# Performance work log

Hardware: AMD Instinct MI355X
Metric: run time of the kernel (lower is better)

The kernel has to match this reference:

```python
import jax, jax.numpy as jnp
import numpy as np

B, T, D, H = 4, 2048, 1024, 16
HD = D // H  # head_size = 64


def setup_inputs() -> dict:
    key = jax.random.key(0)
    ks = jax.random.split(key, 6)
    s = 0.02
    x = jax.random.normal(ks[0], (B, T, D), dtype=jnp.float32)
    # per-head unfused projections, stacked over heads: [H, D, HD]
    Wq = jax.random.normal(ks[1], (H, D, HD), dtype=jnp.float32) * s
    Wk = jax.random.normal(ks[2], (H, D, HD), dtype=jnp.float32) * s
    Wv = jax.random.normal(ks[3], (H, D, HD), dtype=jnp.float32) * s
    # output projection, torch Linear layout [out, in]
    Wo = jax.random.normal(ks[4], (D, D), dtype=jnp.float32) * s
    bo = jax.random.normal(ks[5], (D,), dtype=jnp.float32) * s
    return {"x": x, "Wq": Wq, "Wk": Wk, "Wv": Wv, "Wo": Wo, "bo": bo}


def reference(x, Wq, Wk, Wv, Wo, bo):
    b, t, d = x.shape
    hd = Wq.shape[-1]
    q = jnp.einsum('btd,hdk->bhtk', x, Wq)
    k = jnp.einsum('btd,hdk->bhtk', x, Wk)
    v = jnp.einsum('btd,hdk->bhtk', x, Wv)
    scores = jnp.einsum('bhtk,bhsk->bhts', q, k) / jnp.sqrt(jnp.float32(hd))
    mask = jnp.tril(jnp.ones((t, t), dtype=bool))  # causal
    scores = jnp.where(mask, scores, jnp.float32(-jnp.inf))
    p = jax.nn.softmax(scores, axis=-1)
    o = jnp.einsum('bhts,bhsk->bhtk', p, v)
    o = o.transpose(0, 2, 1, 3).reshape(b, t, d)  # concat heads
    return o @ Wo.T + bo
```

## Files before the change

### kernel.cpp

```cpp
#include <hip/hip_runtime.h>
#include <hip/hip_bf16.h>
#include <stdint.h>

#define B_   4
#define T_   2048
#define D_   1024
#define H_   16
#define HD_  64
#define MROWS (B_*T_)
#define NQKV  3072
#define NST  (T_/64)

typedef __attribute__((ext_vector_type(8))) short  short8;
typedef __attribute__((ext_vector_type(4))) short  bf16x4;
typedef __attribute__((ext_vector_type(4))) float  floatx4;

#define QSCALE 0.1803368801111244f

__device__ inline void async_copy16(const __hip_bfloat16* g, __hip_bfloat16* l) {
  __builtin_amdgcn_global_load_lds(
      (const __attribute__((address_space(1))) void*)g,
      (__attribute__((address_space(3))) void*)l, 16, 0, 0);
}

__device__ inline floatx4 mfma16(bf16x4 a, bf16x4 b, floatx4 c) {
#if __has_builtin(__builtin_amdgcn_mfma_f32_16x16x16bf16_1k)
  return __builtin_amdgcn_mfma_f32_16x16x16bf16_1k(a, b, c, 0, 0, 0);
#elif __has_builtin(__builtin_amdgcn_mfma_f32_16x16x16_bf16)
  return __builtin_amdgcn_mfma_f32_16x16x16_bf16(a, b, c, 0, 0, 0);
#else
  short8 a8 = (short8){a[0], a[1], a[2], a[3], 0, 0, 0, 0};
  short8 b8 = (short8){b[0], b[1], b[2], b[3], 0, 0, 0, 0};
  return __builtin_amdgcn_mfma_f32_16x16x32_bf16(a8, b8, c, 0, 0, 0);
#endif
}


__global__ void convert_bf16(const float* __restrict__ in, __hip_bfloat16* __restrict__ out, int n) {
  int i = (blockIdx.x * blockDim.x + threadIdx.x) * 4;
  if (i < n) {
    float4 v = *(const float4*)(in + i);
    out[i + 0] = __float2bfloat16(v.x);
    out[i + 1] = __float2bfloat16(v.y);
    out[i + 2] = __float2bfloat16(v.z);
    out[i + 3] = __float2bfloat16(v.w);
  }
}

__global__ void transpose_w(const float* __restrict__ Wq, const float* __restrict__ Wk,
                            const float* __restrict__ Wv, __hip_bfloat16* __restrict__ wqkv) {
  __shared__ __hip_bfloat16 tile[64][65];
  const int t = threadIdx.x;
  const int d0 = blockIdx.x * 64;
  const int wh = blockIdx.y;
  const int which = wh >> 4, h = wh & 15;
  const float* W = (which == 0) ? Wq : ((which == 1) ? Wk : Wv);
  const float* base = W + (size_t)h * D_ * HD_;
#pragma unroll
  for (int i = 0; i < 16; i++) {
    int e = i * 256 + t;
    int dr = e >> 6, hd = e & 63;
    tile[dr][hd] = __float2bfloat16(base[(size_t)(d0 + dr) * HD_ + hd]);
  }
  __syncthreads();
#pragma unroll
  for (int i = 0; i < 16; i++) {
    int e = i * 256 + t;
    int hd = e >> 6, dr = e & 63;
    wqkv[(size_t)(which * 1024 + h * 64 + hd) * D_ + d0 + dr] = tile[dr][hd];
  }
}

__global__ void repack_kv(const __hip_bfloat16* __restrict__ qkv,
                          __hip_bfloat16* __restrict__ kpack, __hip_bfloat16* __restrict__ vpack) {
  __shared__ __hip_bfloat16 Ks[64][72];
  __shared__ __hip_bfloat16 Vs[64][72];
  const int tid = threadIdx.x;
  const int st = blockIdx.x, bh = blockIdx.y;
  const int b = bh >> 4, h = bh & 15;
#pragma unroll
  for (int p = 0; p < 2; p++) {
    int c = p * 256 + tid;
    int row = c >> 3, col8 = c & 7;
    const __hip_bfloat16* src = qkv + (size_t)(b * T_ + st * 64 + row) * NQKV + h * HD_ + col8 * 8;
    *(uint4*)&Ks[row][col8 * 8] = *(const uint4*)(src + 1024);
    *(uint4*)&Vs[row][col8 * 8] = *(const uint4*)(src + 2048);
  }
  __syncthreads();
  const size_t base = ((size_t)bh * NST + st) * 8 * 512;
#pragma unroll
  for (int p = 0; p < 2; p++) {
    int pair = p * 256 + tid;
    int c = pair >> 6, l = pair & 63;
    int lq = l & 15, q = l >> 4;
    int ni = c >> 1, half = c & 1;
    short8 v = *(const short8*)&Ks[ni * 16 + lq][half * 32 + q * 8];
    *(short8*)(kpack + base + (size_t)c * 512 + l * 8) = v;
  }
#pragma unroll
  for (int p = 0; p < 2; p++) {
    int pair = p * 256 + tid;
    int c = pair >> 6, l = pair & 63;
    int lq = l & 15, q = l >> 4;
    int m = c >> 2, nt = c & 3;
    __hip_bfloat16 tmp[8];
#pragma unroll
    for (int half = 0; half < 2; half++)
#pragma unroll
      for (int j = 0; j < 4; j++)
        tmp[half * 4 + j] = Vs[(2 * m + half) * 16 + q * 4 + j][nt * 16 + lq];
    *(short8*)(vpack + base + (size_t)c * 512 + l * 8) = *(short8*)tmp;
  }
}

template <int EPI>
__launch_bounds__(256, 2)
__global__ void gemm_bt(const __hip_bfloat16* __restrict__ A, const __hip_bfloat16* __restrict__ Bt,
                        __hip_bfloat16* __restrict__ Cb, float* __restrict__ Cf,
                        const float* __restrict__ bias, int M, int N, int K, float qscale) {
  __shared__ __hip_bfloat16 As[128 * 32];
  __shared__ __hip_bfloat16 Bs[128 * 32];
  const int tid = threadIdx.x;
  const int w = tid >> 6, lane = tid & 63;
  const int lq = lane & 15, quad = lane >> 4;
  const int wr = w >> 1, wc = w & 1;
  const int m0 = blockIdx.x * 128, n0 = blockIdx.y * 128;

  floatx4 acc[4][4];
#pragma unroll
  for (int i = 0; i < 4; i++)
#pragma unroll
    for (int j = 0; j < 4; j++) acc[i][j] = (floatx4){0.f, 0.f, 0.f, 0.f};

  for (int k0 = 0; k0 < K; k0 += 32) {
    __syncthreads();
#pragma unroll
    for (int ph = 0; ph < 2; ++ph) {
      int c = ph * 256 + tid;
      int row = c >> 2, col8 = c & 3;
      async_copy16(A + (size_t)(m0 + row) * K + k0 + col8 * 8, As + c * 8);
      async_copy16(Bt + (size_t)(n0 + row) * K + k0 + col8 * 8, Bs + c * 8);
    }
    __syncthreads();
    short8 af[4], bf[4];
#pragma unroll
    for (int mi = 0; mi < 4; mi++)
      af[mi] = *(const short8*)(As + (wr * 64 + mi * 16 + lq) * 32 + quad * 8);
#pragma unroll
    for (int ni = 0; ni < 4; ni++)
      bf[ni] = *(const short8*)(Bs + (wc * 64 + ni * 16 + lq) * 32 + quad * 8);
#pragma unroll
    for (int mi = 0; mi < 4; mi++)
#pragma unroll
      for (int ni = 0; ni < 4; ni++)
        acc[mi][ni] = __builtin_amdgcn_mfma_f32_16x16x32_bf16(af[mi], bf[ni], acc[mi][ni], 0, 0, 0);
  }

#pragma unroll
  for (int mi = 0; mi < 4; mi++) {
#pragma unroll
    for (int ni = 0; ni < 4; ni++) {
      int col = n0 + wc * 64 + ni * 16 + lq;
      if (EPI == 0) {
        float s = (col < 1024) ? qscale : 1.0f;
#pragma unroll
        for (int r = 0; r < 4; r++) {
          int row = m0 + wr * 64 + mi * 16 + quad * 4 + r;
          Cb[(size_t)row * N + col] = __float2bfloat16(acc[mi][ni][r] * s);
        }
      } else {
        float bv = bias[col];
#pragma unroll
        for (int r = 0; r < 4; r++) {
          int row = m0 + wr * 64 + mi * 16 + quad * 4 + r;
          Cf[(size_t)row * N + col] = acc[mi][ni][r] + bv;
        }
      }
    }
  }
}

__launch_bounds__(256, 4)
__global__ void attn(const __hip_bfloat16* __restrict__ qkv,
                     const __hip_bfloat16* __restrict__ kpack,
                     const __hip_bfloat16* __restrict__ vpack,
                     __hip_bfloat16* __restrict__ obuf) {
  const int tid = threadIdx.x;
  const int w = tid >> 6, lane = tid & 63;
  const int lq = lane & 15, quad = lane >> 4;

  const int L = (int)(blockIdx.x + gridDim.x * blockIdx.y);
  const int bh = (L & 7) * 8 + ((L >> 3) & 7);
  const int qpair = L >> 6;
  const int b = bh >> 4, h = bh & 15;

  const __hip_bfloat16* kb0 = kpack + ((size_t)bh * NST) * 4096 + lane * 8;
  const __hip_bfloat16* vb0 = vpack + ((size_t)bh * NST) * 4096 + lane * 8;

#pragma unroll 1
  for (int seg = 0; seg < 2; ++seg) {
    const int qt = seg ? (NST - 1 - qpair) : qpair;
    const int qt0 = qt * 64;

    short8 qf0, qf1;
    {
      const __hip_bfloat16* qp = qkv + ((size_t)(b * T_ + qt0 + w * 16 + lq)) * NQKV + h * HD_;
      qf0 = *(const short8*)(qp + quad * 8);
      qf1 = *(const short8*)(qp + 32 + quad * 8);
    }

    floatx4 Oacc[4];
#pragma unroll
    for (int i = 0; i < 4; i++) Oacc[i] = (floatx4){0.f, 0.f, 0.f, 0.f};
    float lrow = 0.f;

    const __hip_bfloat16* kb = kb0;
    const __hip_bfloat16* vb = vb0;
    const int nIter = qt + 1;
    for (int it = 0; it < nIter; ++it) {
      short8 kf[4], kg[4];
#pragma unroll
      for (int ni = 0; ni < 4; ni++) {
        kf[ni] = *(const short8*)(kb + (size_t)(ni * 2 + 0) * 512);
        kg[ni] = *(const short8*)(kb + (size_t)(ni * 2 + 1) * 512);
      }
      short8 vfr[8];
#pragma unroll
      for (int c = 0; c < 8; c++) vfr[c] = *(const short8*)(vb + (size_t)c * 512);

      floatx4 Sc[4];
#pragma unroll
      for (int ni = 0; ni < 4; ni++) {
        floatx4 c0 = (floatx4){0.f, 0.f, 0.f, 0.f};
        c0 = __builtin_amdgcn_mfma_f32_16x16x32_bf16(kf[ni], qf0, c0, 0, 0, 0);
        c0 = __builtin_amdgcn_mfma_f32_16x16x32_bf16(kg[ni], qf1, c0, 0, 0, 0);
        Sc[ni] = c0;
      }

      if (it == nIter - 1) {
#pragma unroll
        for (int ni = 0; ni < 4; ni++)
#pragma unroll
          for (int r = 0; r < 4; r++) {
            int s_loc = ni * 16 + quad * 4 + r;
            if (s_loc > w * 16 + lq) Sc[ni][r] = -__builtin_inff();
          }
      }

      bf16x4 pf[4];
#pragma unroll
      for (int c = 0; c < 4; c++) {
        __hip_bfloat16 pb[4];
#pragma unroll
        for (int r = 0; r < 4; r++) {
          float p = __builtin_amdgcn_exp2f(Sc[c][r]);
          lrow += p;
          pb[r] = __float2bfloat16(p);
        }
        pf[c] = *(bf16x4*)pb;
      }

#pragma unroll
      for (int m = 0; m < 2; m++)
#pragma unroll
        for (int nt = 0; nt < 4; nt++) {
          short8 v8 = vfr[m * 4 + nt];
          bf16x4 vlo = (bf16x4){v8[0], v8[1], v8[2], v8[3]};
          bf16x4 vhi = (bf16x4){v8[4], v8[5], v8[6], v8[7]};
          Oacc[nt] = mfma16(pf[2 * m + 0], vlo, Oacc[nt]);
          Oacc[nt] = mfma16(pf[2 * m + 1], vhi, Oacc[nt]);
        }

      kb += 4096;
      vb += 4096;
    }

    float ps = lrow;
    ps += __shfl_xor(ps, 16);
    ps += __shfl_xor(ps, 32);
    float inv = 1.0f / ps;
#pragma unroll
    for (int r = 0; r < 4; r++) {
      float invr = __shfl(inv, quad * 4 + r);
      int t = qt0 + w * 16 + quad * 4 + r;
#pragma unroll
      for (int nt = 0; nt < 4; nt++)
        obuf[(size_t)(b * T_ + t) * D_ + h * HD_ + nt * 16 + lq] =
            __float2bfloat16(Oacc[nt][r] * invr);
    }
  }
}


extern "C" void kernel_launch(void* const* d_in, const int* in_sizes, int n_in,
                              void* d_out, int out_size, void* d_ws, size_t ws_size,
                              hipStream_t stream) {
  const float* x  = (const float*)d_in[0];
  const float* Wq = (const float*)d_in[1];
  const float* Wk = (const float*)d_in[2];
  const float* Wv = (const float*)d_in[3];
  const float* Wo = (const float*)d_in[4];
  const float* bo = (const float*)d_in[5];
  float* out = (float*)d_out;

  char* ws = (char*)d_ws;
  __hip_bfloat16* xb    = (__hip_bfloat16*)(ws);
  __hip_bfloat16* obuf  = (__hip_bfloat16*)(ws);
  __hip_bfloat16* wqkv  = (__hip_bfloat16*)(ws + ((size_t)16 << 20));
  __hip_bfloat16* wob   = (__hip_bfloat16*)(ws + ((size_t)22 << 20));
  __hip_bfloat16* qkv   = (__hip_bfloat16*)(ws + ((size_t)24 << 20));
  __hip_bfloat16* kpack = (__hip_bfloat16*)(ws + ((size_t)72 << 20));
  __hip_bfloat16* vpack = (__hip_bfloat16*)(ws + ((size_t)88 << 20));

  convert_bf16<<<(MROWS * D_) / 1024, 256, 0, stream>>>(x, xb, MROWS * D_);
  convert_bf16<<<(D_ * D_) / 1024, 256, 0, stream>>>(Wo, wob, D_ * D_);
  transpose_w<<<dim3(16, 48), 256, 0, stream>>>(Wq, Wk, Wv, wqkv);

  gemm_bt<0><<<dim3(MROWS / 128, NQKV / 128), 256, 0, stream>>>(
      xb, wqkv, qkv, nullptr, nullptr, MROWS, NQKV, D_, QSCALE);

  repack_kv<<<dim3(NST, B_ * H_), 256, 0, stream>>>(qkv, kpack, vpack);

  attn<<<dim3(NST / 2, B_ * H_), 256, 0, stream>>>(qkv, kpack, vpack, obuf);

  gemm_bt<1><<<dim3(MROWS / 128, D_ / 128), 256, 0, stream>>>(
      obuf, wob, nullptr, out, bo, MROWS, D_, D_, 1.0f);
}
```

Baseline: 267.7 us.

## Give each attention wave two 16-row query blocks to reuse K/V fragments

Each wave now handles 32 query rows (two 16-row blocks) instead of 16, so every K/V fragment loaded from global memory feeds twice as many MFMAs. A block covers two adjacent 64-row query tiles, one per wave pair, instead of a front/back pair of tiles processed in sequence. This drops the causal load-balancing pairing and the bh swizzle, and reverses blockIdx.x so the longest tiles launch first. Register pressure rises, so the launch bound is lowered from 4 to 3 waves per SIMD, and the two wave pairs in a block now do unequal work.

Result: slower. 292.5 us (+9.2%).

```diff
diff --git a/kernel.cpp b/kernel.cpp
--- a/kernel.cpp
+++ b/kernel.cpp
@@ -180,7 +180,7 @@
   }
 }
 
-__launch_bounds__(256, 4)
+__launch_bounds__(256, 3)
 __global__ void attn(const __hip_bfloat16* __restrict__ qkv,
                      const __hip_bfloat16* __restrict__ kpack,
                      const __hip_bfloat16* __restrict__ vpack,
@@ -189,104 +189,115 @@
   const int w = tid >> 6, lane = tid & 63;
   const int lq = lane & 15, quad = lane >> 4;
 
-  const int L = (int)(blockIdx.x + gridDim.x * blockIdx.y);
-  const int bh = (L & 7) * 8 + ((L >> 3) & 7);
-  const int qpair = L >> 6;
+  const int j = 15 - (int)blockIdx.x;
+  const int bh = blockIdx.y;
   const int b = bh >> 4, h = bh & 15;
-
-  const __hip_bfloat16* kb0 = kpack + ((size_t)bh * NST) * 4096 + lane * 8;
-  const __hip_bfloat16* vb0 = vpack + ((size_t)bh * NST) * 4096 + lane * 8;
-
-#pragma unroll 1
-  for (int seg = 0; seg < 2; ++seg) {
-    const int qt = seg ? (NST - 1 - qpair) : qpair;
-    const int qt0 = qt * 64;
-
-    short8 qf0, qf1;
-    {
-      const __hip_bfloat16* qp = qkv + ((size_t)(b * T_ + qt0 + w * 16 + lq)) * NQKV + h * HD_;
-      qf0 = *(const short8*)(qp + quad * 8);
-      qf1 = *(const short8*)(qp + 32 + quad * 8);
-    }
-
-    floatx4 Oacc[4];
-#pragma unroll
-    for (int i = 0; i < 4; i++) Oacc[i] = (floatx4){0.f, 0.f, 0.f, 0.f};
-    float lrow = 0.f;
-
-    const __hip_bfloat16* kb = kb0;
-    const __hip_bfloat16* vb = vb0;
-    const int nIter = qt + 1;
-    for (int it = 0; it < nIter; ++it) {
-      short8 kf[4], kg[4];
-#pragma unroll
-      for (int ni = 0; ni < 4; ni++) {
-        kf[ni] = *(const short8*)(kb + (size_t)(ni * 2 + 0) * 512);
-        kg[ni] = *(const short8*)(kb + (size_t)(ni * 2 + 1) * 512);
-      }
-      short8 vfr[8];
-#pragma unroll
-      for (int c = 0; c < 8; c++) vfr[c] = *(const short8*)(vb + (size_t)c * 512);
-
-      floatx4 Sc[4];
+  const int qt = 2 * j + (w >> 1);
+  const int rbase = (w & 1) * 32;
+
+  short8 qf[2][2];
+#pragma unroll
+  for (int bi = 0; bi < 2; bi++) {
+    const __hip_bfloat16* qp =
+        qkv + ((size_t)(b * T_ + qt * 64 + rbase + bi * 16 + lq)) * NQKV + h * HD_;
+    qf[bi][0] = *(const short8*)(qp + quad * 8);
+    qf[bi][1] = *(const short8*)(qp + 32 + quad * 8);
+  }
+
+  floatx4 Oacc[2][4];
+#pragma unroll
+  for (int bi = 0; bi < 2; bi++)
+#pragma unroll
+    for (int i = 0; i < 4; i++) Oacc[bi][i] = (floatx4){0.f, 0.f, 0.f, 0.f};
+  float lrow[2] = {0.f, 0.f};
+
+  const __hip_bfloat16* kb = kpack + ((size_t)bh * NST) * 4096 + lane * 8;
+  const __hip_bfloat16* vb = vpack + ((size_t)bh * NST) * 4096 + lane * 8;
+
+  const int nIter = qt + 1;
+  for (int it = 0; it < nIter; ++it) {
+    short8 kf[4], kg[4];
+#pragma unroll
+    for (int ni = 0; ni < 4; ni++) {
+      kf[ni] = *(const short8*)(kb + (size_t)(ni * 2 + 0) * 512);
+      kg[ni] = *(const short8*)(kb + (size_t)(ni * 2 + 1) * 512);
+    }
+    short8 vfr[8];
+#pragma unroll
+    for (int c = 0; c < 8; c++) vfr[c] = *(const short8*)(vb + (size_t)c * 512);
+
+    floatx4 Sc[2][4];
+#pragma unroll
+    for (int bi = 0; bi < 2; bi++)
 #pragma unroll
       for (int ni = 0; ni < 4; ni++) {
         floatx4 c0 = (floatx4){0.f, 0.f, 0.f, 0.f};
-        c0 = __builtin_amdgcn_mfma_f32_16x16x32_bf16(kf[ni], qf0, c0, 0, 0, 0);
-        c0 = __builtin_amdgcn_mfma_f32_16x16x32_bf16(kg[ni], qf1, c0, 0, 0, 0);
-        Sc[ni] = c0;
-      }
-
-      if (it == nIter - 1) {
+        c0 = __builtin_amdgcn_mfma_f32_16x16x32_bf16(kf[ni], qf[bi][0], c0, 0, 0, 0);
+        c0 = __builtin_amdgcn_mfma_f32_16x16x32_bf16(kg[ni], qf[bi][1], c0, 0, 0, 0);
+        Sc[bi][ni] = c0;
+      }
+
+    if (it == nIter - 1) {
+#pragma unroll
+      for (int bi = 0; bi < 2; bi++) {
+        int lrow_idx = rbase + bi * 16 + lq;
 #pragma unroll
         for (int ni = 0; ni < 4; ni++)
 #pragma unroll
           for (int r = 0; r < 4; r++) {
             int s_loc = ni * 16 + quad * 4 + r;
-            if (s_loc > w * 16 + lq) Sc[ni][r] = -__builtin_inff();
+            if (s_loc > lrow_idx) Sc[bi][ni][r] = -__builtin_inff();
           }
       }
-
-      bf16x4 pf[4];
+    }
+
+    bf16x4 pf[2][4];
+#pragma unroll
+    for (int bi = 0; bi < 2; bi++)
 #pragma unroll
       for (int c = 0; c < 4; c++) {
         __hip_bfloat16 pb[4];
 #pragma unroll
         for (int r = 0; r < 4; r++) {
-          float p = __builtin_amdgcn_exp2f(Sc[c][r]);
-          lrow += p;
+          float p = __builtin_amdgcn_exp2f(Sc[bi][c][r]);
+          lrow[bi] += p;
           pb[r] = __float2bfloat16(p);
         }
-        pf[c] = *(bf16x4*)pb;
-      }
-
-#pragma unroll
-      for (int m = 0; m < 2; m++)
-#pragma unroll
-        for (int nt = 0; nt < 4; nt++) {
-          short8 v8 = vfr[m * 4 + nt];
-          bf16x4 vlo = (bf16x4){v8[0], v8[1], v8[2], v8[3]};
-          bf16x4 vhi = (bf16x4){v8[4], v8[5], v8[6], v8[7]};
-          Oacc[nt] = mfma16(pf[2 * m + 0], vlo, Oacc[nt]);
-          Oacc[nt] = mfma16(pf[2 * m + 1], vhi, Oacc[nt]);
+        pf[bi][c] = *(bf16x4*)pb;
+      }
+
+#pragma unroll
+    for (int m = 0; m < 2; m++)
+#pragma unroll
+      for (int nt = 0; nt < 4; nt++) {
+        short8 v8 = vfr[m * 4 + nt];
+        bf16x4 vlo = (bf16x4){v8[0], v8[1], v8[2], v8[3]};
+        bf16x4 vhi = (bf16x4){v8[4], v8[5], v8[6], v8[7]};
+#pragma unroll
+        for (int bi = 0; bi < 2; bi++) {
+          Oacc[bi][nt] = mfma16(pf[bi][2 * m + 0], vlo, Oacc[bi][nt]);
+          Oacc[bi][nt] = mfma16(pf[bi][2 * m + 1], vhi, Oacc[bi][nt]);
         }
-
-      kb += 4096;
-      vb += 4096;
-    }
-
-    float ps = lrow;
+      }
+
+    kb += 4096;
+    vb += 4096;
+  }
+
+#pragma unroll
+  for (int bi = 0; bi < 2; bi++) {
+    float ps = lrow[bi];
     ps += __shfl_xor(ps, 16);
     ps += __shfl_xor(ps, 32);
     float inv = 1.0f / ps;
 #pragma unroll
     for (int r = 0; r < 4; r++) {
       float invr = __shfl(inv, quad * 4 + r);
-      int t = qt0 + w * 16 + quad * 4 + r;
+      int t = qt * 64 + rbase + bi * 16 + quad * 4 + r;
 #pragma unroll
       for (int nt = 0; nt < 4; nt++)
         obuf[(size_t)(b * T_ + t) * D_ + h * HD_ + nt * 16 + lq] =
-            __float2bfloat16(Oacc[nt][r] * invr);
+            __float2bfloat16(Oacc[bi][nt][r] * invr);
     }
   }
 }
@@ -321,7 +332,7 @@
 
   repack_kv<<<dim3(NST, B_ * H_), 256, 0, stream>>>(qkv, kpack, vpack);
 
-  attn<<<dim3(NST / 2, B_ * H_), 256, 0, stream>>>(qkv, kpack, vpack, obuf);
+  attn<<<dim3(16, B_ * H_), 256, 0, stream>>>(qkv, kpack, vpack, obuf);
 
   gemm_bt<1><<<dim3(MROWS / 128, D_ / 128), 256, 0, stream>>>(
       obuf, wob, nullptr, out, bo, MROWS, D_, D_, 1.0f);
```
